# Optimization experiments

Measured on AMD Instinct MI355X. Metric: run time of the kernel, lower is better.

## Reference

```python
import jax, jax.numpy as jnp
import numpy as np

N_CHANNELS = 1024
N_HEADS = 16
SEQ = 2048
BATCH = 2


def setup_inputs() -> dict:
    key = jax.random.key(0)
    k1, k2, k3 = jax.random.split(key, 3)
    x = jax.random.normal(k1, (BATCH, SEQ, N_CHANNELS), dtype=jnp.float32)
    qkv_w = jax.random.normal(k2, (3 * N_CHANNELS, N_CHANNELS), dtype=jnp.float32) * 0.02
    qkv_b = jnp.zeros((3 * N_CHANNELS,), dtype=jnp.float32)
    proj_w = jax.random.normal(k3, (N_CHANNELS, N_CHANNELS), dtype=jnp.float32) * 0.02
    proj_b = jnp.zeros((N_CHANNELS,), dtype=jnp.float32)
    return {"x": x, "qkv_w": qkv_w, "qkv_b": qkv_b, "proj_w": proj_w, "proj_b": proj_b}


def reference(x, qkv_w, qkv_b, proj_w, proj_b):
    bs, t, c = x.shape
    h = N_HEADS
    hd = c // h
    scale = hd ** (-0.5)
    # qkv projection: torch Linear is x @ W^T + b
    qkv = x @ qkv_w.T + qkv_b  # [B, T, 3C]
    qkv = qkv.reshape(bs, t, 3, h, hd)
    q, k, v = qkv[:, :, 0], qkv[:, :, 1], qkv[:, :, 2]  # each [B, T, H, hd]
    logits = jnp.einsum('bthc,bshc->bhts', q, k) * scale  # [B, H, T, T]
    # causal mask: log(tril(ones)) -> 0 below diag, -inf above
    causal = jnp.tril(jnp.ones((t, t), dtype=bool))
    logits = jnp.where(causal[None, None], logits, -jnp.inf)
    attn = jax.nn.softmax(logits, axis=-1)
    out = jnp.einsum('bhts,bshc->bthc', attn, v).reshape(bs, t, c)
    out = out @ proj_w.T + proj_b
    return out
```

## Files before the change

### kernel.cpp

```cpp
#include <hip/hip_runtime.h>

typedef __bf16 bf16x8 __attribute__((ext_vector_type(8)));
typedef float f32x4 __attribute__((ext_vector_type(4)));

__device__ inline ushort f2bf(float f) {
    unsigned u = __builtin_bit_cast(unsigned, f);
    unsigned r = (u + 0x7FFFu + ((u >> 16) & 1u)) >> 16;
    return (ushort)r;
}
__device__ inline uint4 pack8(const float* f) {
    uint4 r;
    r.x = (unsigned)f2bf(f[0]) | ((unsigned)f2bf(f[1]) << 16);
    r.y = (unsigned)f2bf(f[2]) | ((unsigned)f2bf(f[3]) << 16);
    r.z = (unsigned)f2bf(f[4]) | ((unsigned)f2bf(f[5]) << 16);
    r.w = (unsigned)f2bf(f[6]) | ((unsigned)f2bf(f[7]) << 16);
    return r;
}

#define MFMA_BF16(a, b, c) __builtin_amdgcn_mfma_f32_16x16x32_bf16(a, b, c, 0, 0, 0)
#define GLDS(g, l) __builtin_amdgcn_global_load_lds( \
    (const __attribute__((address_space(1))) void*)(g), \
    (__attribute__((address_space(3))) void*)(l), 16, 0, 0)

#define QSCALE 0.18033688011112042f

__global__ __launch_bounds__(256) void convert3(
    const float* __restrict__ s0, ushort* __restrict__ d0,
    const float* __restrict__ s1, ushort* __restrict__ d1,
    const float* __restrict__ s2, ushort* __restrict__ d2)
{
    const int i = blockIdx.x * 256 + threadIdx.x;
    const float* s; ushort* d; int off;
    if (i < 524288)      { s = s0; d = d0; off = i; }
    else if (i < 917504) { s = s1; d = d1; off = i - 524288; }
    else                 { s = s2; d = d2; off = i - 917504; }
    const float4* f = (const float4*)s + off * 2;
    float fa[8];
    *(float4*)&fa[0] = f[0];
    *(float4*)&fa[4] = f[1];
    ((uint4*)d)[off] = pack8(fa);
}

template <int MODE>
__global__ __launch_bounds__(256) void gemm128(
    const ushort* __restrict__ A, const ushort* __restrict__ B,
    const float* __restrict__ bias, float* __restrict__ outD,
    ushort* __restrict__ outQ, ushort* __restrict__ outK, ushort* __restrict__ outV,
    int N, int K)
{
    __shared__ __align__(16) ushort SMEM[17408];
    ushort* As = SMEM;
    ushort* Bs = SMEM + 8192;

    const int tid = threadIdx.x;
    const int w = tid >> 6;
    const int lane = tid & 63;
    const int l15 = lane & 15;
    const int quad = lane >> 4;
    const int m0 = blockIdx.x * 128;
    const int n0 = blockIdx.y * 128;
    const int wr = (w & 1) * 64;
    const int wc = (w >> 1) * 64;

    f32x4 acc[4][4] = {};

    for (int k0 = 0; k0 < K; k0 += 64) {
        __syncthreads();
#pragma unroll
        for (int j = 0; j < 4; j++) {
            const int r0 = w * 32 + j * 8;
            const int row = r0 + (lane >> 3);
            const int gcol = ((lane & 7) ^ (row & 7)) * 8;
            GLDS(A + (size_t)(m0 + row) * K + k0 + gcol, As + r0 * 64);
            GLDS(B + (size_t)(n0 + row) * K + k0 + gcol, Bs + r0 * 64);
        }
        __syncthreads();

        bf16x8 af[4][2], bf[4][2];
#pragma unroll
        for (int i = 0; i < 4; i++)
#pragma unroll
            for (int kk = 0; kk < 2; kk++) {
                const int ra = wr + i * 16 + l15;
                const int rb = wc + i * 16 + l15;
                const int ua = ((kk * 4 + quad) ^ (ra & 7)) * 8;
                const int ub = ((kk * 4 + quad) ^ (rb & 7)) * 8;
                af[i][kk] = *(const bf16x8*)&As[ra * 64 + ua];
                bf[i][kk] = *(const bf16x8*)&Bs[rb * 64 + ub];
            }
#pragma unroll
        for (int kk = 0; kk < 2; kk++)
#pragma unroll
            for (int mi = 0; mi < 4; mi++)
#pragma unroll
                for (int ni = 0; ni < 4; ni++)
                    acc[mi][ni] = MFMA_BF16(af[mi][kk], bf[ni][kk], acc[mi][ni]);
    }

    if (MODE == 0) {
        const int which = n0 >> 10;
        ushort* Ct = SMEM;
        __syncthreads();
        if (which == 2) {
#pragma unroll
            for (int mi = 0; mi < 4; mi++)
#pragma unroll
                for (int ni = 0; ni < 4; ni++)
#pragma unroll
                    for (int r = 0; r < 4; r++) {
                        const int m_loc = wr + mi * 16 + quad * 4 + r;
                        const int n_loc = wc + ni * 16 + l15;
                        Ct[n_loc * 136 + m_loc] =
                            f2bf(acc[mi][ni][r] + bias[n0 + n_loc]);
                    }
            __syncthreads();
            const int b = m0 >> 11;
#pragma unroll
            for (int i = 0; i < 8; i++) {
                const int vi = tid + i * 256;
                const int n_loc = vi >> 4, mblk = vi & 15;
                const uint4 val = *(const uint4*)&Ct[n_loc * 136 + mblk * 8];
                const int t = (m0 & 2047) + mblk * 8;
                const int c = (n0 + n_loc) & 1023;
                const int h = c >> 6, d = c & 63;
                *(uint4*)&outV[((size_t)(b * 16 + h) * 64 + d) * 2048 + t] = val;
            }
        } else {
            const float qs = (which == 0) ? QSCALE : 1.0f;
#pragma unroll
            for (int mi = 0; mi < 4; mi++)
#pragma unroll
                for (int ni = 0; ni < 4; ni++)
#pragma unroll
                    for (int r = 0; r < 4; r++) {
                        const int m_loc = wr + mi * 16 + quad * 4 + r;
                        const int n_loc = wc + ni * 16 + l15;
                        Ct[m_loc * 136 + n_loc] =
                            f2bf((acc[mi][ni][r] + bias[n0 + n_loc]) * qs);
                    }
            __syncthreads();
            ushort* outP = (which == 0) ? outQ : outK;
            const int hb = (n0 & 1023) >> 6;
            const int b = m0 >> 11;
#pragma unroll
            for (int i = 0; i < 8; i++) {
                const int vi = tid + i * 256;
                const int m_loc = vi >> 4, u = vi & 15;
                const uint4 val = *(const uint4*)&Ct[m_loc * 136 + u * 8];
                const int t = (m0 & 2047) + m_loc;
                const int h = hb + (u >> 3);
                const int d8 = (u & 7) * 8;
                *(uint4*)&outP[((size_t)(b * 16 + h)) * 131072 + (size_t)t * 64 + d8] = val;
            }
        }
        return;
    }

    float* Cf = (float*)SMEM;
#pragma unroll
    for (int cch = 0; cch < 2; cch++) {
        __syncthreads();
        if ((wc >> 6) == cch) {
#pragma unroll
            for (int mi = 0; mi < 4; mi++)
#pragma unroll
                for (int ni = 0; ni < 4; ni++)
#pragma unroll
                    for (int r = 0; r < 4; r++) {
                        const int m_loc = wr + mi * 16 + quad * 4 + r;
                        const int nl = ni * 16 + l15;
                        Cf[m_loc * 68 + nl] =
                            acc[mi][ni][r] + bias[n0 + cch * 64 + nl];
                    }
        }
        __syncthreads();
#pragma unroll
        for (int i = 0; i < 8; i++) {
            const int vi = tid + i * 256;
            const int m_loc = vi >> 4, u = vi & 15;
            const float4 val = *(const float4*)&Cf[m_loc * 68 + u * 4];
            const int m = m0 + m_loc;
            const int n = n0 + cch * 64 + u * 4;
            *(float4*)&outD[(size_t)m * N + n] = val;
        }
    }
}

__global__ __launch_bounds__(256) void attn2(
    const ushort* __restrict__ Q, const ushort* __restrict__ K,
    const ushort* __restrict__ Vt, ushort* __restrict__ O)
{
    __shared__ __align__(16) ushort KV[2][2][64 * 64];
    __shared__ __align__(16) __bf16 Ps[4][16 * 72];

    const int bh = blockIdx.x;
    const int qt = 31 - blockIdx.y;
    const int q0 = qt * 64;
    const int tid = threadIdx.x;
    const int w = tid >> 6;
    const int lane = tid & 63;
    const int l15 = lane & 15;
    const int quad = lane >> 4;

    auto stage = [&](int kt, int b) {
        const int t0 = kt * 64;
#pragma unroll
        for (int j = 0; j < 2; j++) {
            const int r0 = w * 16 + j * 8;
            const int row = r0 + (lane >> 3);
            const int gcol = ((lane & 7) ^ (row & 7)) * 8;
            GLDS(K + ((size_t)bh * 2048 + t0 + row) * 64 + gcol, &KV[b][0][r0 * 64]);
            GLDS(Vt + ((size_t)bh * 64 + row) * 2048 + t0 + gcol, &KV[b][1][r0 * 64]);
        }
    };

    const ushort* qbase = Q + ((size_t)bh * 2048 + q0 + w * 16 + l15) * 64;
    bf16x8 qf0 = *(const bf16x8*)(qbase + quad * 8);
    bf16x8 qf1 = *(const bf16x8*)(qbase + 32 + quad * 8);

    bf16x8 ones;
#pragma unroll
    for (int j = 0; j < 8; j++) ones[j] = (__bf16)1.0f;

    f32x4 oacc[4] = {};
    f32x4 lacc = {};

    stage(0, 0);

    for (int kt = 0; kt <= qt; kt++) {
        __syncthreads();
        if (kt < qt) stage(kt + 1, (kt + 1) & 1);

        const ushort* Ks = &KV[kt & 1][0][0];
        const ushort* Vs = &KV[kt & 1][1][0];
        const int t0 = kt * 64;

        f32x4 sacc[4] = {};
#pragma unroll
        for (int cb = 0; cb < 4; cb++) {
            const int rr = cb * 16 + l15;
            bf16x8 b0 = *(const bf16x8*)&Ks[rr * 64 + ((quad ^ (rr & 7)) * 8)];
            bf16x8 b1 = *(const bf16x8*)&Ks[rr * 64 + (((4 + quad) ^ (rr & 7)) * 8)];
            sacc[cb] = MFMA_BF16(qf0, b0, sacc[cb]);
            sacc[cb] = MFMA_BF16(qf1, b1, sacc[cb]);
        }

        __bf16* pw = &Ps[w][0];
        __builtin_amdgcn_wave_barrier();
        if (kt == qt) {
#pragma unroll
            for (int cb = 0; cb < 4; cb++)
#pragma unroll
                for (int r = 0; r < 4; r++) {
                    const int col = t0 + cb * 16 + l15;
                    const int row = q0 + w * 16 + quad * 4 + r;
                    const float x = (col > row) ? -1e30f : sacc[cb][r];
                    pw[(quad * 4 + r) * 72 + cb * 16 + l15] =
                        (__bf16)__builtin_exp2f(x);
                }
        } else {
#pragma unroll
            for (int cb = 0; cb < 4; cb++)
#pragma unroll
                for (int r = 0; r < 4; r++)
                    pw[(quad * 4 + r) * 72 + cb * 16 + l15] =
                        (__bf16)__builtin_exp2f(sacc[cb][r]);
        }
        __builtin_amdgcn_s_waitcnt(0xC07F);
        __builtin_amdgcn_wave_barrier();

#pragma unroll
        for (int kc = 0; kc < 2; kc++) {
            bf16x8 afr = *(const bf16x8*)&pw[l15 * 72 + kc * 32 + quad * 8];
#pragma unroll
            for (int cb = 0; cb < 4; cb++) {
                const int rr = cb * 16 + l15;
                bf16x8 bfr = *(const bf16x8*)&Vs[rr * 64 + (((kc * 4 + quad) ^ (rr & 7)) * 8)];
                oacc[cb] = MFMA_BF16(afr, bfr, oacc[cb]);
            }
            lacc = MFMA_BF16(afr, ones, lacc);
        }
    }

    const int b = bh >> 4, h = bh & 15;
#pragma unroll
    for (int r = 0; r < 4; r++) {
        const float inv = 1.0f / lacc[r];
        const int row = q0 + w * 16 + quad * 4 + r;
#pragma unroll
        for (int cb = 0; cb < 4; cb++) {
            const int col = h * 64 + cb * 16 + l15;
            O[((size_t)b * 2048 + row) * 1024 + col] = f2bf(oacc[cb][r] * inv);
        }
    }
}

extern "C" void kernel_launch(void* const* d_in, const int* in_sizes, int n_in,
                              void* d_out, int out_size, void* d_ws, size_t ws_size,
                              hipStream_t stream) {
    const float* x      = (const float*)d_in[0];
    const float* qkv_w  = (const float*)d_in[1];
    const float* qkv_b  = (const float*)d_in[2];
    const float* proj_w = (const float*)d_in[3];
    const float* proj_b = (const float*)d_in[4];

    ushort* XbOb  = (ushort*)d_ws + 16;
    ushort* Wqkv  = XbOb + 4194304;
    ushort* Wproj = Wqkv + 3145728;
    ushort* Qb    = Wproj + 1048576;
    ushort* Kb    = Qb + 4194304;
    ushort* Vt    = Kb + 4194304;

    convert3<<<4096, 256, 0, stream>>>(x, XbOb, qkv_w, Wqkv, proj_w, Wproj);
    gemm128<0><<<dim3(32, 24), 256, 0, stream>>>(XbOb, Wqkv, qkv_b, nullptr,
                                                 Qb, Kb, Vt, 3072, 1024);
    attn2<<<dim3(32, 32), 256, 0, stream>>>(Qb, Kb, Vt, XbOb);
    gemm128<1><<<dim3(32, 8), 256, 0, stream>>>(XbOb, Wproj, proj_b, (float*)d_out,
                                                nullptr, nullptr, nullptr, 1024, 1024);
}
```

Measured before the change: 201.8 us.

## Enlarge attention query tile to 128 rows and shrink projection GEMM tile

The attention kernel now handles 128 query rows per block, with each wave owning 32 rows, so every K/V tile staged in LDS feeds twice as many MFMAs and the grid halves to 512 blocks. The causal mask is now applied per wave based on its row range. Separately, the output projection gets its own 64x128-tile GEMM with 512 blocks instead of 256, giving better CU coverage on the small GEMM. The trade-offs are more registers per attention wave and fewer, longer attention blocks, which may worsen load balance across the causal triangle.

Result: slower. 209.8 us (+4.0%).

```diff
diff --git a/kernel.cpp b/kernel.cpp
--- a/kernel.cpp
+++ b/kernel.cpp
@@ -41,10 +41,9 @@
     ((uint4*)d)[off] = pack8(fa);
 }
 
-template <int MODE>
-__global__ __launch_bounds__(256) void gemm128(
+__global__ __launch_bounds__(256) void gemm_qkv(
     const ushort* __restrict__ A, const ushort* __restrict__ B,
-    const float* __restrict__ bias, float* __restrict__ outD,
+    const float* __restrict__ bias,
     ushort* __restrict__ outQ, ushort* __restrict__ outK, ushort* __restrict__ outV,
     int N, int K)
 {
@@ -97,63 +96,123 @@
                     acc[mi][ni] = MFMA_BF16(af[mi][kk], bf[ni][kk], acc[mi][ni]);
     }
 
-    if (MODE == 0) {
-        const int which = n0 >> 10;
-        ushort* Ct = SMEM;
-        __syncthreads();
-        if (which == 2) {
-#pragma unroll
-            for (int mi = 0; mi < 4; mi++)
+    const int which = n0 >> 10;
+    ushort* Ct = SMEM;
+    __syncthreads();
+    if (which == 2) {
+#pragma unroll
+        for (int mi = 0; mi < 4; mi++)
+#pragma unroll
+            for (int ni = 0; ni < 4; ni++)
+#pragma unroll
+                for (int r = 0; r < 4; r++) {
+                    const int m_loc = wr + mi * 16 + quad * 4 + r;
+                    const int n_loc = wc + ni * 16 + l15;
+                    Ct[n_loc * 136 + m_loc] =
+                        f2bf(acc[mi][ni][r] + bias[n0 + n_loc]);
+                }
+        __syncthreads();
+        const int b = m0 >> 11;
+#pragma unroll
+        for (int i = 0; i < 8; i++) {
+            const int vi = tid + i * 256;
+            const int n_loc = vi >> 4, mblk = vi & 15;
+            const uint4 val = *(const uint4*)&Ct[n_loc * 136 + mblk * 8];
+            const int t = (m0 & 2047) + mblk * 8;
+            const int c = (n0 + n_loc) & 1023;
+            const int h = c >> 6, d = c & 63;
+            *(uint4*)&outV[((size_t)(b * 16 + h) * 64 + d) * 2048 + t] = val;
+        }
+    } else {
+        const float qs = (which == 0) ? QSCALE : 1.0f;
+#pragma unroll
+        for (int mi = 0; mi < 4; mi++)
+#pragma unroll
+            for (int ni = 0; ni < 4; ni++)
+#pragma unroll
+                for (int r = 0; r < 4; r++) {
+                    const int m_loc = wr + mi * 16 + quad * 4 + r;
+                    const int n_loc = wc + ni * 16 + l15;
+                    Ct[m_loc * 136 + n_loc] =
+                        f2bf((acc[mi][ni][r] + bias[n0 + n_loc]) * qs);
+                }
+        __syncthreads();
+        ushort* outP = (which == 0) ? outQ : outK;
+        const int hb = (n0 & 1023) >> 6;
+        const int b = m0 >> 11;
+#pragma unroll
+        for (int i = 0; i < 8; i++) {
+            const int vi = tid + i * 256;
+            const int m_loc = vi >> 4, u = vi & 15;
+            const uint4 val = *(const uint4*)&Ct[m_loc * 136 + u * 8];
+            const int t = (m0 & 2047) + m_loc;
+            const int h = hb + (u >> 3);
+            const int d8 = (u & 7) * 8;
+            *(uint4*)&outP[((size_t)(b * 16 + h)) * 131072 + (size_t)t * 64 + d8] = val;
+        }
+    }
+}
+
+__global__ __launch_bounds__(256) void gemm_proj(
+    const ushort* __restrict__ A, const ushort* __restrict__ B,
+    const float* __restrict__ bias, float* __restrict__ outD)
+{
+    const int N = 1024, K = 1024;
+    __shared__ __align__(16) ushort SMEM[12288];
+    ushort* As = SMEM;
+    ushort* Bs = SMEM + 4096;
+
+    const int tid = threadIdx.x;
+    const int w = tid >> 6;
+    const int lane = tid & 63;
+    const int l15 = lane & 15;
+    const int quad = lane >> 4;
+    const int m0 = blockIdx.x * 64;
+    const int n0 = blockIdx.y * 128;
+    const int wr = (w & 1) * 32;
+    const int wc = (w >> 1) * 64;
+
+    f32x4 acc[2][4] = {};
+
+    for (int k0 = 0; k0 < K; k0 += 64) {
+        __syncthreads();
+#pragma unroll
+        for (int j = 0; j < 2; j++) {
+            const int r0 = w * 16 + j * 8;
+            const int row = r0 + (lane >> 3);
+            const int gcol = ((lane & 7) ^ (row & 7)) * 8;
+            GLDS(A + (size_t)(m0 + row) * K + k0 + gcol, As + r0 * 64);
+        }
+#pragma unroll
+        for (int j = 0; j < 4; j++) {
+            const int r0 = w * 32 + j * 8;
+            const int row = r0 + (lane >> 3);
+            const int gcol = ((lane & 7) ^ (row & 7)) * 8;
+            GLDS(B + (size_t)(n0 + row) * K + k0 + gcol, Bs + r0 * 64);
+        }
+        __syncthreads();
+
+        bf16x8 af[2][2], bf[4][2];
+#pragma unroll
+        for (int kk = 0; kk < 2; kk++) {
+#pragma unroll
+            for (int mi = 0; mi < 2; mi++) {
+                const int ra = wr + mi * 16 + l15;
+                af[mi][kk] = *(const bf16x8*)&As[ra * 64 + (((kk * 4 + quad) ^ (ra & 7)) * 8)];
+            }
+#pragma unroll
+            for (int ni = 0; ni < 4; ni++) {
+                const int rb = wc + ni * 16 + l15;
+                bf[ni][kk] = *(const bf16x8*)&Bs[rb * 64 + (((kk * 4 + quad) ^ (rb & 7)) * 8)];
+            }
+        }
+#pragma unroll
+        for (int kk = 0; kk < 2; kk++)
+#pragma unroll
+            for (int mi = 0; mi < 2; mi++)
 #pragma unroll
                 for (int ni = 0; ni < 4; ni++)
-#pragma unroll
-                    for (int r = 0; r < 4; r++) {
-                        const int m_loc = wr + mi * 16 + quad * 4 + r;
-                        const int n_loc = wc + ni * 16 + l15;
-                        Ct[n_loc * 136 + m_loc] =
-                            f2bf(acc[mi][ni][r] + bias[n0 + n_loc]);
-                    }
-            __syncthreads();
-            const int b = m0 >> 11;
-#pragma unroll
-            for (int i = 0; i < 8; i++) {
-                const int vi = tid + i * 256;
-                const int n_loc = vi >> 4, mblk = vi & 15;
-                const uint4 val = *(const uint4*)&Ct[n_loc * 136 + mblk * 8];
-                const int t = (m0 & 2047) + mblk * 8;
-                const int c = (n0 + n_loc) & 1023;
-                const int h = c >> 6, d = c & 63;
-                *(uint4*)&outV[((size_t)(b * 16 + h) * 64 + d) * 2048 + t] = val;
-            }
-        } else {
-            const float qs = (which == 0) ? QSCALE : 1.0f;
-#pragma unroll
-            for (int mi = 0; mi < 4; mi++)
-#pragma unroll
-                for (int ni = 0; ni < 4; ni++)
-#pragma unroll
-                    for (int r = 0; r < 4; r++) {
-                        const int m_loc = wr + mi * 16 + quad * 4 + r;
-                        const int n_loc = wc + ni * 16 + l15;
-                        Ct[m_loc * 136 + n_loc] =
-                            f2bf((acc[mi][ni][r] + bias[n0 + n_loc]) * qs);
-                    }
-            __syncthreads();
-            ushort* outP = (which == 0) ? outQ : outK;
-            const int hb = (n0 & 1023) >> 6;
-            const int b = m0 >> 11;
-#pragma unroll
-            for (int i = 0; i < 8; i++) {
-                const int vi = tid + i * 256;
-                const int m_loc = vi >> 4, u = vi & 15;
-                const uint4 val = *(const uint4*)&Ct[m_loc * 136 + u * 8];
-                const int t = (m0 & 2047) + m_loc;
-                const int h = hb + (u >> 3);
-                const int d8 = (u & 7) * 8;
-                *(uint4*)&outP[((size_t)(b * 16 + h)) * 131072 + (size_t)t * 64 + d8] = val;
-            }
-        }
-        return;
+                    acc[mi][ni] = MFMA_BF16(af[mi][kk], bf[ni][kk], acc[mi][ni]);
     }
 
     float* Cf = (float*)SMEM;
@@ -162,40 +221,37 @@
         __syncthreads();
         if ((wc >> 6) == cch) {
 #pragma unroll
-            for (int mi = 0; mi < 4; mi++)
+            for (int mi = 0; mi < 2; mi++)
 #pragma unroll
                 for (int ni = 0; ni < 4; ni++)
 #pragma unroll
                     for (int r = 0; r < 4; r++) {
                         const int m_loc = wr + mi * 16 + quad * 4 + r;
                         const int nl = ni * 16 + l15;
-                        Cf[m_loc * 68 + nl] =
-                            acc[mi][ni][r] + bias[n0 + cch * 64 + nl];
+                        Cf[m_loc * 68 + nl] = acc[mi][ni][r] + bias[n0 + cch * 64 + nl];
                     }
         }
         __syncthreads();
 #pragma unroll
-        for (int i = 0; i < 8; i++) {
+        for (int i = 0; i < 4; i++) {
             const int vi = tid + i * 256;
             const int m_loc = vi >> 4, u = vi & 15;
             const float4 val = *(const float4*)&Cf[m_loc * 68 + u * 4];
-            const int m = m0 + m_loc;
-            const int n = n0 + cch * 64 + u * 4;
-            *(float4*)&outD[(size_t)m * N + n] = val;
-        }
-    }
-}
-
-__global__ __launch_bounds__(256) void attn2(
+            *(float4*)&outD[(size_t)(m0 + m_loc) * N + n0 + cch * 64 + u * 4] = val;
+        }
+    }
+}
+
+__global__ __launch_bounds__(256) void attn3(
     const ushort* __restrict__ Q, const ushort* __restrict__ K,
     const ushort* __restrict__ Vt, ushort* __restrict__ O)
 {
     __shared__ __align__(16) ushort KV[2][2][64 * 64];
-    __shared__ __align__(16) __bf16 Ps[4][16 * 72];
+    __shared__ __align__(16) __bf16 Ps[4][32 * 72];
 
     const int bh = blockIdx.x;
-    const int qt = 31 - blockIdx.y;
-    const int q0 = qt * 64;
+    const int qt = 15 - blockIdx.y;
+    const int q0 = qt * 128;
     const int tid = threadIdx.x;
     const int w = tid >> 6;
     const int lane = tid & 63;
@@ -214,85 +270,106 @@
         }
     };
 
-    const ushort* qbase = Q + ((size_t)bh * 2048 + q0 + w * 16 + l15) * 64;
-    bf16x8 qf0 = *(const bf16x8*)(qbase + quad * 8);
-    bf16x8 qf1 = *(const bf16x8*)(qbase + 32 + quad * 8);
+    bf16x8 qf[2][2];
+#pragma unroll
+    for (int mi = 0; mi < 2; mi++) {
+        const ushort* qb = Q + ((size_t)bh * 2048 + q0 + w * 32 + mi * 16 + l15) * 64;
+        qf[mi][0] = *(const bf16x8*)(qb + quad * 8);
+        qf[mi][1] = *(const bf16x8*)(qb + 32 + quad * 8);
+    }
 
     bf16x8 ones;
 #pragma unroll
     for (int j = 0; j < 8; j++) ones[j] = (__bf16)1.0f;
 
-    f32x4 oacc[4] = {};
-    f32x4 lacc = {};
+    f32x4 oacc[2][4] = {};
+    f32x4 lacc[2] = {};
 
     stage(0, 0);
-
-    for (int kt = 0; kt <= qt; kt++) {
-        __syncthreads();
-        if (kt < qt) stage(kt + 1, (kt + 1) & 1);
+    const int ktmax = 2 * qt + 1;
+
+    for (int kt = 0; kt <= ktmax; kt++) {
+        __syncthreads();
+        if (kt < ktmax) stage(kt + 1, (kt + 1) & 1);
 
         const ushort* Ks = &KV[kt & 1][0][0];
         const ushort* Vs = &KV[kt & 1][1][0];
         const int t0 = kt * 64;
 
-        f32x4 sacc[4] = {};
+        f32x4 sacc[2][4] = {};
 #pragma unroll
         for (int cb = 0; cb < 4; cb++) {
             const int rr = cb * 16 + l15;
             bf16x8 b0 = *(const bf16x8*)&Ks[rr * 64 + ((quad ^ (rr & 7)) * 8)];
             bf16x8 b1 = *(const bf16x8*)&Ks[rr * 64 + (((4 + quad) ^ (rr & 7)) * 8)];
-            sacc[cb] = MFMA_BF16(qf0, b0, sacc[cb]);
-            sacc[cb] = MFMA_BF16(qf1, b1, sacc[cb]);
+#pragma unroll
+            for (int mi = 0; mi < 2; mi++) {
+                sacc[mi][cb] = MFMA_BF16(qf[mi][0], b0, sacc[mi][cb]);
+                sacc[mi][cb] = MFMA_BF16(qf[mi][1], b1, sacc[mi][cb]);
+            }
         }
 
         __bf16* pw = &Ps[w][0];
         __builtin_amdgcn_wave_barrier();
-        if (kt == qt) {
-#pragma unroll
-            for (int cb = 0; cb < 4; cb++)
-#pragma unroll
-                for (int r = 0; r < 4; r++) {
-                    const int col = t0 + cb * 16 + l15;
-                    const int row = q0 + w * 16 + quad * 4 + r;
-                    const float x = (col > row) ? -1e30f : sacc[cb][r];
-                    pw[(quad * 4 + r) * 72 + cb * 16 + l15] =
-                        (__bf16)__builtin_exp2f(x);
-                }
+        if (t0 + 63 > q0 + w * 32) {
+#pragma unroll
+            for (int mi = 0; mi < 2; mi++)
+#pragma unroll
+                for (int cb = 0; cb < 4; cb++)
+#pragma unroll
+                    for (int r = 0; r < 4; r++) {
+                        const int col = t0 + cb * 16 + l15;
+                        const int row = q0 + w * 32 + mi * 16 + quad * 4 + r;
+                        const float x = (col > row) ? -1e30f : sacc[mi][cb][r];
+                        pw[(mi * 16 + quad * 4 + r) * 72 + cb * 16 + l15] =
+                            (__bf16)__builtin_exp2f(x);
+                    }
         } else {
 #pragma unroll
-            for (int cb = 0; cb < 4; cb++)
-#pragma unroll
-                for (int r = 0; r < 4; r++)
-                    pw[(quad * 4 + r) * 72 + cb * 16 + l15] =
-                        (__bf16)__builtin_exp2f(sacc[cb][r]);
+            for (int mi = 0; mi < 2; mi++)
+#pragma unroll
+                for (int cb = 0; cb < 4; cb++)
+#pragma unroll
+                    for (int r = 0; r < 4; r++)
+                        pw[(mi * 16 + quad * 4 + r) * 72 + cb * 16 + l15] =
+                            (__bf16)__builtin_exp2f(sacc[mi][cb][r]);
         }
         __builtin_amdgcn_s_waitcnt(0xC07F);
         __builtin_amdgcn_wave_barrier();
 
 #pragma unroll
         for (int kc = 0; kc < 2; kc++) {
-            bf16x8 afr = *(const bf16x8*)&pw[l15 * 72 + kc * 32 + quad * 8];
+            bf16x8 afr[2];
+#pragma unroll
+            for (int mi = 0; mi < 2; mi++)
+                afr[mi] = *(const bf16x8*)&pw[(mi * 16 + l15) * 72 + kc * 32 + quad * 8];
 #pragma unroll
             for (int cb = 0; cb < 4; cb++) {
                 const int rr = cb * 16 + l15;
                 bf16x8 bfr = *(const bf16x8*)&Vs[rr * 64 + (((kc * 4 + quad) ^ (rr & 7)) * 8)];
-                oacc[cb] = MFMA_BF16(afr, bfr, oacc[cb]);
-            }
-            lacc = MFMA_BF16(afr, ones, lacc);
+#pragma unroll
+                for (int mi = 0; mi < 2; mi++)
+                    oacc[mi][cb] = MFMA_BF16(afr[mi], bfr, oacc[mi][cb]);
+            }
+#pragma unroll
+            for (int mi = 0; mi < 2; mi++)
+                lacc[mi] = MFMA_BF16(afr[mi], ones, lacc[mi]);
         }
     }
 
     const int b = bh >> 4, h = bh & 15;
 #pragma unroll
-    for (int r = 0; r < 4; r++) {
-        const float inv = 1.0f / lacc[r];
-        const int row = q0 + w * 16 + quad * 4 + r;
-#pragma unroll
-        for (int cb = 0; cb < 4; cb++) {
-            const int col = h * 64 + cb * 16 + l15;
-            O[((size_t)b * 2048 + row) * 1024 + col] = f2bf(oacc[cb][r] * inv);
-        }
-    }
+    for (int mi = 0; mi < 2; mi++)
+#pragma unroll
+        for (int r = 0; r < 4; r++) {
+            const float inv = 1.0f / lacc[mi][r];
+            const int row = q0 + w * 32 + mi * 16 + quad * 4 + r;
+#pragma unroll
+            for (int cb = 0; cb < 4; cb++) {
+                const int col = h * 64 + cb * 16 + l15;
+                O[((size_t)b * 2048 + row) * 1024 + col] = f2bf(oacc[mi][cb][r] * inv);
+            }
+        }
 }
 
 extern "C" void kernel_launch(void* const* d_in, const int* in_sizes, int n_in,
@@ -312,9 +389,8 @@
     ushort* Vt    = Kb + 4194304;
 
     convert3<<<4096, 256, 0, stream>>>(x, XbOb, qkv_w, Wqkv, proj_w, Wproj);
-    gemm128<0><<<dim3(32, 24), 256, 0, stream>>>(XbOb, Wqkv, qkv_b, nullptr,
-                                                 Qb, Kb, Vt, 3072, 1024);
-    attn2<<<dim3(32, 32), 256, 0, stream>>>(Qb, Kb, Vt, XbOb);
-    gemm128<1><<<dim3(32, 8), 256, 0, stream>>>(XbOb, Wproj, proj_b, (float*)d_out,
-                                                nullptr, nullptr, nullptr, 1024, 1024);
-}
+    gemm_qkv<<<dim3(32, 24), 256, 0, stream>>>(XbOb, Wqkv, qkv_b,
+                                               Qb, Kb, Vt, 3072, 1024);
+    attn3<<<dim3(32, 16), 256, 0, stream>>>(Qb, Kb, Vt, XbOb);
+    gemm_proj<<<dim3(64, 8), 256, 0, stream>>>(XbOb, Wproj, proj_b, (float*)d_out);
+}
```
